# Performance work log

Measured on AMD Instinct MI355X. Metric: run time of the kernel, lower is better.

The kernel has to match this reference:

```python
import jax, jax.numpy as jnp
import numpy as np

NU = 8192   # num_users
NI = 8192   # num_items
B = 4096    # batch_size
D = 64      # embed_size
NS = 5      # num_scores


def _w(key, fan_in, fan_out):
    # xavier-uniform-like init
    lim = np.sqrt(6.0 / (fan_in + fan_out)).astype(np.float32)
    return jax.random.uniform(key, (fan_in, fan_out), jnp.float32, -lim, lim)


def setup_inputs() -> dict:
    key = jax.random.key(0)
    ks = jax.random.split(key, 32)
    z = lambda n: jnp.zeros((n,), jnp.float32)
    inp = {
        "batch_user": jax.random.randint(ks[0], (B,), 0, NU),
        "batch_item": jax.random.randint(ks[1], (B,), 0, NI),
        "R": jax.random.uniform(ks[2], (NU, NI), jnp.float32),
        "S": jax.random.uniform(ks[3], (NU, NU), jnp.float32),
        "U": _w(ks[4], NU, D),
        "V": _w(ks[5], NI, D),
        "w_r": _w(ks[6], NS, D), "b_r": z(D),
        "Wu0": _w(ks[7], 2 * D, D), "bu0": z(D), "Wu1": _w(ks[8], D, D), "bu1": z(D),
        "Wv0": _w(ks[9], 2 * D, D), "bv0": z(D), "Wv1": _w(ks[10], D, D), "bv1": z(D),
        "Wc0": _w(ks[11], 2 * D, D), "bc0": z(D), "Wc1": _w(ks[12], D, D), "bc1": z(D),
        "Wg0": _w(ks[13], 2 * D, D), "bg0": z(D), "Wg1": _w(ks[14], D, D), "bg1": z(D),
        "W_I": _w(ks[15], D, D), "b_I": z(D),
        "W_Sm": _w(ks[16], D, D), "b_Sm": z(D),
        "W1A": _w(ks[17], 2 * D, D), "b1A": z(D), "w2A": _w(ks[18], D, 1), "b2A": z(1),
        "W1B": _w(ks[19], 2 * D, D), "b1B": z(D), "w2B": _w(ks[20], D, 1), "b2B": z(1),
        "W1M": _w(ks[21], 2 * D, D), "b1M": z(D), "w2M": _w(ks[22], D, 1), "b2M": z(1),
        "W_Z": _w(ks[23], D, D), "b_Z": z(D),
    }
    return inp


def reference(batch_user, batch_item, R, S, U, V, w_r, b_r,
              Wu0, bu0, Wu1, bu1, Wv0, bv0, Wv1, bv1,
              Wc0, bc0, Wc1, bc1, Wg0, bg0, Wg1, bg1,
              W_I, b_I, W_Sm, b_Sm,
              W1A, b1A, w2A, b2A, W1B, b1B, w2B, b2B,
              W1M, b1M, w2M, b2M, W_Z, b_Z):
    relu = jax.nn.relu
    # rating embedding: e_r = Linear(num_scores->d) applied to vector [1..num_scores]
    e_r = jnp.arange(1, w_r.shape[0] + 1, dtype=w_r.dtype) @ w_r + b_r  # [d]
    Uc = jnp.concatenate([U, jnp.broadcast_to(e_r, U.shape)], axis=1)  # [NU, 2d]
    Vc = jnp.concatenate([V, jnp.broadcast_to(e_r, V.shape)], axis=1)  # [NI, 2d]
    # per-node MLP stacks (num_layer=2; layer0: 2d->d, layer1: d->d)
    Uh = relu(relu(Uc @ Wu0 + bu0) @ Wu1 + bu1)  # [NU, d]
    Vh = relu(relu(Vc @ Wv0 + bv0) @ Wv1 + bv1)  # [NI, d]
    Ub = Uh[batch_user]  # [B, d]
    Vb = Vh[batch_item]  # [B, d]
    # item-space attention A over batch, softmax along batch dim
    A = jax.nn.softmax(relu(jnp.concatenate([Vb, Ub], axis=1) @ W1A + b1A) @ w2A + b2A, axis=0)  # [B,1]
    # attention-weighted sparse-row aggregation over item embeddings
    H_I = relu(((R[batch_user] * A) @ Vh) @ W_I + b_I)  # [B, d]
    Bw = jax.nn.softmax(relu(jnp.concatenate([H_I, Ub], axis=1) @ W1B + b1B) @ w2B + b2B, axis=0)  # [B,1]
    H_S = relu(((S[batch_user] * Bw) @ Uh) @ W_Sm + b_Sm)  # [B, d]
    H = jnp.concatenate([H_I, H_S], axis=1)  # [B, 2d]
    H = relu(relu(H @ Wc0 + bc0) @ Wc1 + bc1)  # [B, d]
    M = jax.nn.softmax(relu(jnp.concatenate([Ub, Vb], axis=1) @ W1M + b1M) @ w2M + b2M, axis=0)  # [B,1]
    # R.T row-gather: columns of R for batch items -> [B, NU]
    Rt_b = jnp.take(R, batch_item, axis=1).T
    Z = relu(((Rt_b * M) @ Uh) @ W_Z + b_Z)  # [B, d]
    G = jnp.concatenate([H, Z], axis=1)  # [B, 2d]
    G = relu(relu(G @ Wg0 + bg0) @ Wg1 + bg1)  # [B, d]
    return G
```

## Files before the change

### kernel.cpp

```cpp
#include <hip/hip_runtime.h>
#include <stdint.h>


typedef short bf16x8 __attribute__((ext_vector_type(8)));
typedef float f32x4 __attribute__((ext_vector_type(4)));

#define NKZ    8
#define KLEN   1024
#define KITERS 32

__device__ __forceinline__ unsigned f2bf1(float f) {
    unsigned x = __float_as_uint(f);
    return (x + 0x7FFFu + ((x >> 16) & 1u)) >> 16;
}

__device__ __forceinline__ float wsum(float v) {
    #pragma unroll
    for (int o = 32; o; o >>= 1) v += __shfl_xor(v, o);
    return v;
}

__device__ __forceinline__ void block_softmax_stats(const float* __restrict__ s,
                                                    float& m, float& inv) {
    __shared__ float r1[4];
    __shared__ float r2[4];
    int t = threadIdx.x, lane = t & 63, wv = t >> 6;
    float lm = -3.4e38f;
    #pragma unroll
    for (int i = 0; i < 16; ++i) lm = fmaxf(lm, s[t + 256 * i]);
    #pragma unroll
    for (int o = 32; o; o >>= 1) lm = fmaxf(lm, __shfl_xor(lm, o));
    if (lane == 0) r1[wv] = lm;
    __syncthreads();
    m = fmaxf(fmaxf(r1[0], r1[1]), fmaxf(r1[2], r1[3]));
    float ls = 0.f;
    #pragma unroll
    for (int i = 0; i < 16; ++i) ls += __expf(s[t + 256 * i] - m);
    ls = wsum(ls);
    if (lane == 0) r2[wv] = ls;
    __syncthreads();
    inv = 1.f / (r2[0] + r2[1] + r2[2] + r2[3]);
}

__global__ __launch_bounds__(256) void k_mlp(
    const float* __restrict__ U, const float* __restrict__ V,
    const float* __restrict__ w_r, const float* __restrict__ b_r,
    const float* __restrict__ Wu0, const float* __restrict__ bu0,
    const float* __restrict__ Wu1, const float* __restrict__ bu1,
    const float* __restrict__ Wv0, const float* __restrict__ bv0,
    const float* __restrict__ Wv1, const float* __restrict__ bv1,
    float* __restrict__ Uh, float* __restrict__ Vh,
    unsigned short* __restrict__ Uhb, unsigned short* __restrict__ Vhb)
{
    int gt = blockIdx.x * 256 + threadIdx.x;
    int wid = gt >> 6;
    int lane = gt & 63;

    float er = b_r[lane];
    #pragma unroll
    for (int s = 0; s < 5; ++s) er += (float)(s + 1) * w_r[s * 64 + lane];

    const int isV = (wid >= 2048);
    const float* X  = isV ? V   : U;
    const float* W0 = isV ? Wv0 : Wu0;
    const float* B0 = isV ? bv0 : bu0;
    const float* W1 = isV ? Wv1 : Wu1;
    const float* B1 = isV ? bv1 : bu1;
    float* Hout          = isV ? Vh  : Uh;
    unsigned short* Hb   = isV ? Vhb : Uhb;
    int r0 = (wid & 2047) * 4;

    float x[4];
    #pragma unroll
    for (int j = 0; j < 4; ++j) x[j] = X[(r0 + j) * 64 + lane];

    float h0c = B0[lane];
    for (int k = 0; k < 64; ++k) h0c += __shfl(er, k) * W0[(64 + k) * 64 + lane];

    float h0[4];
    #pragma unroll
    for (int j = 0; j < 4; ++j) h0[j] = h0c;
    for (int k = 0; k < 64; ++k) {
        float wv = W0[k * 64 + lane];
        #pragma unroll
        for (int j = 0; j < 4; ++j) h0[j] += __shfl(x[j], k) * wv;
    }
    #pragma unroll
    for (int j = 0; j < 4; ++j) h0[j] = fmaxf(h0[j], 0.f);

    float h1[4];
    #pragma unroll
    for (int j = 0; j < 4; ++j) h1[j] = B1[lane];
    for (int k = 0; k < 64; ++k) {
        float wv = W1[k * 64 + lane];
        #pragma unroll
        for (int j = 0; j < 4; ++j) h1[j] += __shfl(h0[j], k) * wv;
    }
    #pragma unroll
    for (int j = 0; j < 4; ++j) {
        h1[j] = fmaxf(h1[j], 0.f);
        Hout[(r0 + j) * 64 + lane] = h1[j];
    }
    unsigned pw[2];
    #pragma unroll
    for (int q = 0; q < 2; ++q) pw[q] = f2bf1(h1[2*q]) | (f2bf1(h1[2*q+1]) << 16);
    unsigned short* dst = Hb + (size_t)(r0 >> 3) * 512 + (lane >> 4) * 128
                        + (lane & 15) * 8 + (r0 & 7);
    *(uint2*)dst = make_uint2(pw[0], pw[1]);
}

__global__ __launch_bounds__(256) void k_gemmQ(
    const float* __restrict__ R,
    const unsigned short* __restrict__ Uhb,
    float* __restrict__ Qp)
{
    __shared__ float lds[2][2048];
    const int tile = blockIdx.x & 127;
    const int kz   = blockIdx.x >> 7;
    const int i0 = tile * 64;
    const int u0 = kz * KLEN;
    const int t = threadIdx.x;
    const int w = t >> 6, l = t & 63, lg = l >> 4, lr = l & 15;

    f32x4 acc[4] = {};

    const float* gbase = R + ((size_t)u0 + (t >> 4)) * 8192 + i0 + (t & 15) * 4;

    #pragma unroll
    for (int q = 0; q < 2; ++q) {
        const float* g = gbase + (size_t)(q * 16) * 8192;
        __builtin_amdgcn_global_load_lds(
            (const __attribute__((address_space(1))) void*)g,
            (__attribute__((address_space(3))) void*)&lds[0][(q * 256 + t) * 4],
            16, 0, 0);
    }
    __syncthreads();

    const int iloc = w * 16 + lr;
    for (int s = 0; s < KITERS; ++s) {
        if (s + 1 < KITERS) {
            int nb = (s + 1) & 1;
            #pragma unroll
            for (int q = 0; q < 2; ++q) {
                const float* g = gbase + (size_t)((s + 1) * 32 + q * 16) * 8192;
                __builtin_amdgcn_global_load_lds(
                    (const __attribute__((address_space(1))) void*)g,
                    (__attribute__((address_space(3))) void*)&lds[nb][(q * 256 + t) * 4],
                    16, 0, 0);
            }
        }
        const float* Lb = lds[s & 1];
        float av[8];
        #pragma unroll
        for (int j = 0; j < 8; ++j) av[j] = Lb[(8 * lg + j) * 64 + iloc];
        union { bf16x8 v; unsigned u[4]; } af;
        #pragma unroll
        for (int q = 0; q < 4; ++q)
            af.u[q] = f2bf1(av[2*q]) | (f2bf1(av[2*q+1]) << 16);
        const unsigned short* bp = Uhb + (size_t)((u0 >> 3) + s * 4 + lg) * 512 + lr * 8;
        #pragma unroll
        for (int c = 0; c < 4; ++c) {
            bf16x8 bf = *(const bf16x8*)(bp + c * 128);
            acc[c] = __builtin_amdgcn_mfma_f32_16x16x32_bf16(af.v, bf, acc[c], 0, 0, 0);
        }
        __syncthreads();
    }

    float* out = Qp + (size_t)(kz * 8192 + tile * 64 + w * 16 + lg * 4) * 64 + lr;
    #pragma unroll
    for (int c = 0; c < 4; ++c) {
        #pragma unroll
        for (int j = 0; j < 4; ++j) out[j * 64 + c * 16] = acc[c][j];
    }
}

__global__ __launch_bounds__(256) void k_gemmP(
    const float* __restrict__ R, const float* __restrict__ S,
    const int* __restrict__ bu,
    const unsigned short* __restrict__ Uhb, const unsigned short* __restrict__ Vhb,
    float* __restrict__ PpI, float* __restrict__ PpS)
{
    const int gP = NKZ * 64;
    int bid = blockIdx.x;
    const int isS = bid >= gP;
    int q = isS ? bid - gP : bid;
    int tile = q & 63, kz = q >> 6;
    int tid = threadIdx.x;
    int w = tid >> 6, l = tid & 63;
    int lg = l >> 4, lr = l & 15;

    int brow = tile * 64 + w * 16 + lr;
    int ridx = bu[brow];
    const float* A = (isS ? S : R) + (size_t)ridx * 8192 + kz * KLEN + lg * 8;
    const unsigned short* Bb = (isS ? Uhb : Vhb)
                             + (size_t)((kz * KLEN) >> 3) * 512 + lr * 8;

    f32x4 acc[4] = {};
    f32x4 b0[4], b1[4];
    #pragma unroll
    for (int d = 0; d < 4; ++d) {
        b0[d] = ((const f32x4*)(A + d * 32))[0];
        b1[d] = ((const f32x4*)(A + d * 32))[1];
    }

    #pragma unroll 4
    for (int ks = 0; ks < KITERS - 4; ++ks) {
        const int slot = ks & 3;
        union { bf16x8 v; unsigned u[4]; } af;
        af.u[0] = f2bf1(b0[slot].x) | (f2bf1(b0[slot].y) << 16);
        af.u[1] = f2bf1(b0[slot].z) | (f2bf1(b0[slot].w) << 16);
        af.u[2] = f2bf1(b1[slot].x) | (f2bf1(b1[slot].y) << 16);
        af.u[3] = f2bf1(b1[slot].z) | (f2bf1(b1[slot].w) << 16);
        b0[slot] = ((const f32x4*)(A + (ks + 4) * 32))[0];
        b1[slot] = ((const f32x4*)(A + (ks + 4) * 32))[1];
        const unsigned short* bp = Bb + (size_t)(ks * 4 + lg) * 512;
        #pragma unroll
        for (int c = 0; c < 4; ++c) {
            bf16x8 bf = *(const bf16x8*)(bp + c * 128);
            acc[c] = __builtin_amdgcn_mfma_f32_16x16x32_bf16(af.v, bf, acc[c], 0, 0, 0);
        }
    }
    #pragma unroll
    for (int ks = KITERS - 4; ks < KITERS; ++ks) {
        const int slot = ks & 3;
        union { bf16x8 v; unsigned u[4]; } af;
        af.u[0] = f2bf1(b0[slot].x) | (f2bf1(b0[slot].y) << 16);
        af.u[1] = f2bf1(b0[slot].z) | (f2bf1(b0[slot].w) << 16);
        af.u[2] = f2bf1(b1[slot].x) | (f2bf1(b1[slot].y) << 16);
        af.u[3] = f2bf1(b1[slot].z) | (f2bf1(b1[slot].w) << 16);
        const unsigned short* bp = Bb + (size_t)(ks * 4 + lg) * 512;
        #pragma unroll
        for (int c = 0; c < 4; ++c) {
            bf16x8 bf = *(const bf16x8*)(bp + c * 128);
            acc[c] = __builtin_amdgcn_mfma_f32_16x16x32_bf16(af.v, bf, acc[c], 0, 0, 0);
        }
    }

    float* out = (isS ? PpS : PpI)
               + (size_t)(kz * 4096 + tile * 64 + w * 16 + lg * 4) * 64 + lr;
    #pragma unroll
    for (int c = 0; c < 4; ++c) {
        #pragma unroll
        for (int j = 0; j < 4; ++j) out[j * 64 + c * 16] = acc[c][j];
    }
}

__global__ __launch_bounds__(256) void k_scoreAM(
    const int* __restrict__ bu, const int* __restrict__ bi,
    const float* __restrict__ Uh, const float* __restrict__ Vh,
    const float* __restrict__ W1A, const float* __restrict__ b1A,
    const float* __restrict__ w2A, const float* __restrict__ b2A,
    const float* __restrict__ W1M, const float* __restrict__ b1M,
    const float* __restrict__ w2M, const float* __restrict__ b2M,
    float* __restrict__ sA, float* __restrict__ sM)
{
    int gt = blockIdx.x * 256 + threadIdx.x;
    int wid = gt >> 6, lane = gt & 63;
    int b0 = wid * 2;
    float ub[2], vb[2];
    #pragma unroll
    for (int j = 0; j < 2; ++j) {
        ub[j] = Uh[(size_t)bu[b0 + j] * 64 + lane];
        vb[j] = Vh[(size_t)bi[b0 + j] * 64 + lane];
    }
    float hA[2], hM[2];
    #pragma unroll
    for (int j = 0; j < 2; ++j) { hA[j] = b1A[lane]; hM[j] = b1M[lane]; }
    for (int k = 0; k < 64; ++k) {
        float wa0 = W1A[k * 64 + lane], wa1 = W1A[(64 + k) * 64 + lane];
        float wm0 = W1M[k * 64 + lane], wm1 = W1M[(64 + k) * 64 + lane];
        #pragma unroll
        for (int j = 0; j < 2; ++j) {
            float sv = __shfl(vb[j], k), su = __shfl(ub[j], k);
            hA[j] += sv * wa0 + su * wa1;
            hM[j] += su * wm0 + sv * wm1;
        }
    }
    float w2a = w2A[lane], w2m = w2M[lane];
    #pragma unroll
    for (int j = 0; j < 2; ++j) {
        float sa = wsum(fmaxf(hA[j], 0.f) * w2a);
        float sm = wsum(fmaxf(hM[j], 0.f) * w2m);
        if (lane == 0) { sA[b0 + j] = sa + b2A[0]; sM[b0 + j] = sm + b2M[0]; }
    }
}

__global__ __launch_bounds__(256) void k_HI_scoreB(
    const float* __restrict__ PpI, const float* __restrict__ sA,
    const int* __restrict__ bu, const float* __restrict__ Uh,
    const float* __restrict__ W_I, const float* __restrict__ b_I,
    const float* __restrict__ W1B, const float* __restrict__ b1B,
    const float* __restrict__ w2B, const float* __restrict__ b2B,
    float* __restrict__ HI, float* __restrict__ sB)
{
    float m, inv;
    block_softmax_stats(sA, m, inv);
    int wid = blockIdx.x * 4 + (threadIdx.x >> 6);
    int lane = threadIdx.x & 63;
    int b0 = wid * 2;
    float p[2];
    #pragma unroll
    for (int j = 0; j < 2; ++j) {
        int b = b0 + j;
        float a = 0.f;
        #pragma unroll
        for (int kz = 0; kz < NKZ; ++kz)
            a += PpI[(size_t)(kz * 4096 + b) * 64 + lane];
        p[j] = a * (__expf(sA[b] - m) * inv);
    }
    float h[2];
    #pragma unroll
    for (int j = 0; j < 2; ++j) h[j] = b_I[lane];
    for (int k = 0; k < 64; ++k) {
        float wv = W_I[k * 64 + lane];
        #pragma unroll
        for (int j = 0; j < 2; ++j) h[j] += __shfl(p[j], k) * wv;
    }
    float ub[2];
    #pragma unroll
    for (int j = 0; j < 2; ++j) {
        h[j] = fmaxf(h[j], 0.f);
        HI[(size_t)(b0 + j) * 64 + lane] = h[j];
        ub[j] = Uh[(size_t)bu[b0 + j] * 64 + lane];
    }
    float h2[2];
    #pragma unroll
    for (int j = 0; j < 2; ++j) h2[j] = b1B[lane];
    for (int k = 0; k < 64; ++k) {
        float w0 = W1B[k * 64 + lane], w1 = W1B[(64 + k) * 64 + lane];
        #pragma unroll
        for (int j = 0; j < 2; ++j) h2[j] += __shfl(h[j], k) * w0 + __shfl(ub[j], k) * w1;
    }
    float w2 = w2B[lane];
    #pragma unroll
    for (int j = 0; j < 2; ++j) {
        float sv = wsum(fmaxf(h2[j], 0.f) * w2);
        if (lane == 0) sB[b0 + j] = sv + b2B[0];
    }
}

__global__ __launch_bounds__(256) void k_HS_H(
    const float* __restrict__ PpS, const float* __restrict__ sB,
    const float* __restrict__ HI,
    const float* __restrict__ W_Sm, const float* __restrict__ b_Sm,
    const float* __restrict__ Wc0, const float* __restrict__ bc0,
    const float* __restrict__ Wc1, const float* __restrict__ bc1,
    float* __restrict__ Hout)
{
    float m, inv;
    block_softmax_stats(sB, m, inv);
    int wid = blockIdx.x * 4 + (threadIdx.x >> 6);
    int lane = threadIdx.x & 63;
    int b0 = wid * 2;
    float p[2];
    #pragma unroll
    for (int j = 0; j < 2; ++j) {
        int b = b0 + j;
        float a = 0.f;
        #pragma unroll
        for (int kz = 0; kz < NKZ; ++kz)
            a += PpS[(size_t)(kz * 4096 + b) * 64 + lane];
        p[j] = a * (__expf(sB[b] - m) * inv);
    }
    float hs[2];
    #pragma unroll
    for (int j = 0; j < 2; ++j) hs[j] = b_Sm[lane];
    for (int k = 0; k < 64; ++k) {
        float wv = W_Sm[k * 64 + lane];
        #pragma unroll
        for (int j = 0; j < 2; ++j) hs[j] += __shfl(p[j], k) * wv;
    }
    float hi[2];
    #pragma unroll
    for (int j = 0; j < 2; ++j) {
        hs[j] = fmaxf(hs[j], 0.f);
        hi[j] = HI[(size_t)(b0 + j) * 64 + lane];
    }
    float h0[2];
    #pragma unroll
    for (int j = 0; j < 2; ++j) h0[j] = bc0[lane];
    for (int k = 0; k < 64; ++k) {
        float w0 = Wc0[k * 64 + lane], w1 = Wc0[(64 + k) * 64 + lane];
        #pragma unroll
        for (int j = 0; j < 2; ++j) h0[j] += __shfl(hi[j], k) * w0 + __shfl(hs[j], k) * w1;
    }
    #pragma unroll
    for (int j = 0; j < 2; ++j) h0[j] = fmaxf(h0[j], 0.f);
    float h1[2];
    #pragma unroll
    for (int j = 0; j < 2; ++j) h1[j] = bc1[lane];
    for (int k = 0; k < 64; ++k) {
        float wv = Wc1[k * 64 + lane];
        #pragma unroll
        for (int j = 0; j < 2; ++j) h1[j] += __shfl(h0[j], k) * wv;
    }
    #pragma unroll
    for (int j = 0; j < 2; ++j) Hout[(size_t)(b0 + j) * 64 + lane] = fmaxf(h1[j], 0.f);
}

__global__ __launch_bounds__(256) void k_Z_G(
    const float* __restrict__ Qp, const float* __restrict__ sM,
    const int* __restrict__ bi, const float* __restrict__ H,
    const float* __restrict__ W_Z, const float* __restrict__ b_Z,
    const float* __restrict__ Wg0, const float* __restrict__ bg0,
    const float* __restrict__ Wg1, const float* __restrict__ bg1,
    float* __restrict__ G)
{
    float m, inv;
    block_softmax_stats(sM, m, inv);
    int wid = blockIdx.x * 4 + (threadIdx.x >> 6);
    int lane = threadIdx.x & 63;
    int b0 = wid * 2;
    float p[2];
    #pragma unroll
    for (int j = 0; j < 2; ++j) {
        int b = b0 + j;
        int it = bi[b];
        float a = 0.f;
        #pragma unroll
        for (int kz = 0; kz < NKZ; ++kz)
            a += Qp[(size_t)(kz * 8192 + it) * 64 + lane];
        p[j] = a * (__expf(sM[b] - m) * inv);
    }
    float z[2];
    #pragma unroll
    for (int j = 0; j < 2; ++j) z[j] = b_Z[lane];
    for (int k = 0; k < 64; ++k) {
        float wv = W_Z[k * 64 + lane];
        #pragma unroll
        for (int j = 0; j < 2; ++j) z[j] += __shfl(p[j], k) * wv;
    }
    float hr[2];
    #pragma unroll
    for (int j = 0; j < 2; ++j) {
        z[j] = fmaxf(z[j], 0.f);
        hr[j] = H[(size_t)(b0 + j) * 64 + lane];
    }
    float g0[2];
    #pragma unroll
    for (int j = 0; j < 2; ++j) g0[j] = bg0[lane];
    for (int k = 0; k < 64; ++k) {
        float w0 = Wg0[k * 64 + lane], w1 = Wg0[(64 + k) * 64 + lane];
        #pragma unroll
        for (int j = 0; j < 2; ++j) g0[j] += __shfl(hr[j], k) * w0 + __shfl(z[j], k) * w1;
    }
    #pragma unroll
    for (int j = 0; j < 2; ++j) g0[j] = fmaxf(g0[j], 0.f);
    float g1[2];
    #pragma unroll
    for (int j = 0; j < 2; ++j) g1[j] = bg1[lane];
    for (int k = 0; k < 64; ++k) {
        float wv = Wg1[k * 64 + lane];
        #pragma unroll
        for (int j = 0; j < 2; ++j) g1[j] += __shfl(g0[j], k) * wv;
    }
    #pragma unroll
    for (int j = 0; j < 2; ++j) G[(size_t)(b0 + j) * 64 + lane] = fmaxf(g1[j], 0.f);
}

extern "C" void kernel_launch(void* const* d_in, const int* in_sizes, int n_in,
                              void* d_out, int out_size, void* d_ws, size_t ws_size,
                              hipStream_t stream)
{
    (void)in_sizes; (void)n_in; (void)out_size; (void)ws_size;
    const int*   bu  = (const int*)  d_in[0];
    const int*   bi  = (const int*)  d_in[1];
    const float* R   = (const float*)d_in[2];
    const float* S   = (const float*)d_in[3];
    const float* U   = (const float*)d_in[4];
    const float* V   = (const float*)d_in[5];
    const float* w_r = (const float*)d_in[6];
    const float* b_r = (const float*)d_in[7];
    const float* Wu0 = (const float*)d_in[8];
    const float* bu0 = (const float*)d_in[9];
    const float* Wu1 = (const float*)d_in[10];
    const float* bu1 = (const float*)d_in[11];
    const float* Wv0 = (const float*)d_in[12];
    const float* bv0 = (const float*)d_in[13];
    const float* Wv1 = (const float*)d_in[14];
    const float* bv1 = (const float*)d_in[15];
    const float* Wc0 = (const float*)d_in[16];
    const float* bc0 = (const float*)d_in[17];
    const float* Wc1 = (const float*)d_in[18];
    const float* bc1 = (const float*)d_in[19];
    const float* Wg0 = (const float*)d_in[20];
    const float* bg0 = (const float*)d_in[21];
    const float* Wg1 = (const float*)d_in[22];
    const float* bg1 = (const float*)d_in[23];
    const float* W_I = (const float*)d_in[24];
    const float* b_I = (const float*)d_in[25];
    const float* W_Sm= (const float*)d_in[26];
    const float* b_Sm= (const float*)d_in[27];
    const float* W1A = (const float*)d_in[28];
    const float* b1A = (const float*)d_in[29];
    const float* w2A = (const float*)d_in[30];
    const float* b2A = (const float*)d_in[31];
    const float* W1B = (const float*)d_in[32];
    const float* b1B = (const float*)d_in[33];
    const float* w2B = (const float*)d_in[34];
    const float* b2B = (const float*)d_in[35];
    const float* W1M = (const float*)d_in[36];
    const float* b1M = (const float*)d_in[37];
    const float* w2M = (const float*)d_in[38];
    const float* b2M = (const float*)d_in[39];
    const float* W_Z = (const float*)d_in[40];
    const float* b_Z = (const float*)d_in[41];

    char* ws = (char*)d_ws;
    size_t off = 0;
    float*          Uh  = (float*)(ws + off);          off += 2ull << 20;
    float*          Vh  = (float*)(ws + off);          off += 2ull << 20;
    unsigned short* Uhb = (unsigned short*)(ws + off); off += 1ull << 20;
    unsigned short* Vhb = (unsigned short*)(ws + off); off += 1ull << 20;
    float*          PpI = (float*)(ws + off);          off += (size_t)NKZ << 20;
    float*          PpS = (float*)(ws + off);          off += (size_t)NKZ << 20;
    float*          Qp  = (float*)(ws + off);          off += (size_t)(2 * NKZ) << 20;
    float*          sA  = (float*)(ws + off);
    float*          sM  = sA + 4096;
    float*          sB  = sA + 8192;                   off += 3 * 4096 * 4 + 4096;
    float*          HI  = (float*)(ws + off);          off += 1ull << 20;
    float*          Hh  = (float*)(ws + off);

    k_mlp<<<1024, 256, 0, stream>>>(U, V, w_r, b_r, Wu0, bu0, Wu1, bu1,
                                    Wv0, bv0, Wv1, bv1, Uh, Vh, Uhb, Vhb);
    k_gemmQ<<<128 * NKZ, 256, 0, stream>>>(R, Uhb, Qp);
    k_gemmP<<<2 * NKZ * 64, 256, 0, stream>>>(R, S, bu, Uhb, Vhb, PpI, PpS);
    k_scoreAM<<<512, 256, 0, stream>>>(bu, bi, Uh, Vh, W1A, b1A, w2A, b2A,
                                       W1M, b1M, w2M, b2M, sA, sM);
    k_HI_scoreB<<<512, 256, 0, stream>>>(PpI, sA, bu, Uh, W_I, b_I,
                                         W1B, b1B, w2B, b2B, HI, sB);
    k_HS_H<<<512, 256, 0, stream>>>(PpS, sB, HI, W_Sm, b_Sm, Wc0, bc0, Wc1, bc1,
                                    Hh);
    k_Z_G<<<512, 256, 0, stream>>>(Qp, sM, bi, Hh, W_Z, b_Z, Wg0, bg0, Wg1, bg1,
                                   (float*)d_out);
}
```

Before: 224.1 us.

## Merge Q and P GEMMs into one launch with finer split-K

Folds the two split-K GEMM kernels (R^T·Uh over all items, and the gathered R/S rows times Vh/Uh) into one launch that branches on block index. The split-K factor rises from 8 to 16 for the P GEMMs and to 32 for the Q GEMM, and launch bounds request 4 blocks per CU. The intent is more blocks, better occupancy and overlap of the two memory-bound GEMMs, plus one fewer launch. In exchange the partial-sum buffers and the downstream reduction loops grow (Qp becomes 64 MB of partials), which adds write and read traffic.

```diff
diff --git a/kernel.cpp b/kernel.cpp
--- a/kernel.cpp
+++ b/kernel.cpp
@@ -5,9 +5,12 @@
 typedef short bf16x8 __attribute__((ext_vector_type(8)));
 typedef float f32x4 __attribute__((ext_vector_type(4)));
 
-#define NKZ    8
-#define KLEN   1024
-#define KITERS 32
+#define PKZ     16
+#define PKLEN   512
+#define PKITERS 16
+#define QKZ     32
+#define QKLEN   256
+#define QKITERS 8
 
 __device__ __forceinline__ unsigned f2bf1(float f) {
     unsigned x = __float_as_uint(f);
@@ -109,139 +112,132 @@
     *(uint2*)dst = make_uint2(pw[0], pw[1]);
 }
 
-__global__ __launch_bounds__(256) void k_gemmQ(
-    const float* __restrict__ R,
-    const unsigned short* __restrict__ Uhb,
-    float* __restrict__ Qp)
-{
-    __shared__ float lds[2][2048];
-    const int tile = blockIdx.x & 127;
-    const int kz   = blockIdx.x >> 7;
-    const int i0 = tile * 64;
-    const int u0 = kz * KLEN;
-    const int t = threadIdx.x;
-    const int w = t >> 6, l = t & 63, lg = l >> 4, lr = l & 15;
-
-    f32x4 acc[4] = {};
-
-    const float* gbase = R + ((size_t)u0 + (t >> 4)) * 8192 + i0 + (t & 15) * 4;
-
-    #pragma unroll
-    for (int q = 0; q < 2; ++q) {
-        const float* g = gbase + (size_t)(q * 16) * 8192;
-        __builtin_amdgcn_global_load_lds(
-            (const __attribute__((address_space(1))) void*)g,
-            (__attribute__((address_space(3))) void*)&lds[0][(q * 256 + t) * 4],
-            16, 0, 0);
-    }
-    __syncthreads();
-
-    const int iloc = w * 16 + lr;
-    for (int s = 0; s < KITERS; ++s) {
-        if (s + 1 < KITERS) {
-            int nb = (s + 1) & 1;
-            #pragma unroll
-            for (int q = 0; q < 2; ++q) {
-                const float* g = gbase + (size_t)((s + 1) * 32 + q * 16) * 8192;
-                __builtin_amdgcn_global_load_lds(
-                    (const __attribute__((address_space(1))) void*)g,
-                    (__attribute__((address_space(3))) void*)&lds[nb][(q * 256 + t) * 4],
-                    16, 0, 0);
-            }
-        }
-        const float* Lb = lds[s & 1];
-        float av[8];
-        #pragma unroll
-        for (int j = 0; j < 8; ++j) av[j] = Lb[(8 * lg + j) * 64 + iloc];
-        union { bf16x8 v; unsigned u[4]; } af;
-        #pragma unroll
-        for (int q = 0; q < 4; ++q)
-            af.u[q] = f2bf1(av[2*q]) | (f2bf1(av[2*q+1]) << 16);
-        const unsigned short* bp = Uhb + (size_t)((u0 >> 3) + s * 4 + lg) * 512 + lr * 8;
-        #pragma unroll
-        for (int c = 0; c < 4; ++c) {
-            bf16x8 bf = *(const bf16x8*)(bp + c * 128);
-            acc[c] = __builtin_amdgcn_mfma_f32_16x16x32_bf16(af.v, bf, acc[c], 0, 0, 0);
-        }
-        __syncthreads();
-    }
-
-    float* out = Qp + (size_t)(kz * 8192 + tile * 64 + w * 16 + lg * 4) * 64 + lr;
-    #pragma unroll
-    for (int c = 0; c < 4; ++c) {
-        #pragma unroll
-        for (int j = 0; j < 4; ++j) out[j * 64 + c * 16] = acc[c][j];
-    }
-}
-
-__global__ __launch_bounds__(256) void k_gemmP(
+__global__ __launch_bounds__(256, 4) void k_gemm(
     const float* __restrict__ R, const float* __restrict__ S,
     const int* __restrict__ bu,
     const unsigned short* __restrict__ Uhb, const unsigned short* __restrict__ Vhb,
-    float* __restrict__ PpI, float* __restrict__ PpS)
-{
-    const int gP = NKZ * 64;
-    int bid = blockIdx.x;
-    const int isS = bid >= gP;
-    int q = isS ? bid - gP : bid;
-    int tile = q & 63, kz = q >> 6;
-    int tid = threadIdx.x;
-    int w = tid >> 6, l = tid & 63;
-    int lg = l >> 4, lr = l & 15;
-
-    int brow = tile * 64 + w * 16 + lr;
-    int ridx = bu[brow];
-    const float* A = (isS ? S : R) + (size_t)ridx * 8192 + kz * KLEN + lg * 8;
-    const unsigned short* Bb = (isS ? Uhb : Vhb)
-                             + (size_t)((kz * KLEN) >> 3) * 512 + lr * 8;
+    float* __restrict__ PpI, float* __restrict__ PpS, float* __restrict__ Qp)
+{
+    __shared__ float lds[2][2048];
+    const int bid = blockIdx.x;
+    const int t = threadIdx.x;
+    const int w = t >> 6, l = t & 63, lg = l >> 4, lr = l & 15;
 
     f32x4 acc[4] = {};
-    f32x4 b0[4], b1[4];
-    #pragma unroll
-    for (int d = 0; d < 4; ++d) {
-        b0[d] = ((const f32x4*)(A + d * 32))[0];
-        b1[d] = ((const f32x4*)(A + d * 32))[1];
-    }
-
-    #pragma unroll 4
-    for (int ks = 0; ks < KITERS - 4; ++ks) {
-        const int slot = ks & 3;
-        union { bf16x8 v; unsigned u[4]; } af;
-        af.u[0] = f2bf1(b0[slot].x) | (f2bf1(b0[slot].y) << 16);
-        af.u[1] = f2bf1(b0[slot].z) | (f2bf1(b0[slot].w) << 16);
-        af.u[2] = f2bf1(b1[slot].x) | (f2bf1(b1[slot].y) << 16);
-        af.u[3] = f2bf1(b1[slot].z) | (f2bf1(b1[slot].w) << 16);
-        b0[slot] = ((const f32x4*)(A + (ks + 4) * 32))[0];
-        b1[slot] = ((const f32x4*)(A + (ks + 4) * 32))[1];
-        const unsigned short* bp = Bb + (size_t)(ks * 4 + lg) * 512;
+
+    if (bid < 2 * PKZ * 64) {
+        const int gP = PKZ * 64;
+        const int isS = bid >= gP;
+        int q = isS ? bid - gP : bid;
+        int tile = q & 63, kz = q >> 6;
+        int brow = tile * 64 + w * 16 + lr;
+        int ridx = bu[brow];
+        const float* A = (isS ? S : R) + (size_t)ridx * 8192 + kz * PKLEN + lg * 8;
+        const unsigned short* Bb = (isS ? Uhb : Vhb)
+                                 + (size_t)((kz * PKLEN) >> 3) * 512 + lr * 8;
+
+        f32x4 b0[4], b1[4];
+        #pragma unroll
+        for (int d = 0; d < 4; ++d) {
+            b0[d] = ((const f32x4*)(A + d * 32))[0];
+            b1[d] = ((const f32x4*)(A + d * 32))[1];
+        }
+
+        #pragma unroll 4
+        for (int ks = 0; ks < PKITERS - 4; ++ks) {
+            const int slot = ks & 3;
+            union { bf16x8 v; unsigned u[4]; } af;
+            af.u[0] = f2bf1(b0[slot].x) | (f2bf1(b0[slot].y) << 16);
+            af.u[1] = f2bf1(b0[slot].z) | (f2bf1(b0[slot].w) << 16);
+            af.u[2] = f2bf1(b1[slot].x) | (f2bf1(b1[slot].y) << 16);
+            af.u[3] = f2bf1(b1[slot].z) | (f2bf1(b1[slot].w) << 16);
+            b0[slot] = ((const f32x4*)(A + (ks + 4) * 32))[0];
+            b1[slot] = ((const f32x4*)(A + (ks + 4) * 32))[1];
+            const unsigned short* bp = Bb + (size_t)(ks * 4 + lg) * 512;
+            #pragma unroll
+            for (int c = 0; c < 4; ++c) {
+                bf16x8 bf = *(const bf16x8*)(bp + c * 128);
+                acc[c] = __builtin_amdgcn_mfma_f32_16x16x32_bf16(af.v, bf, acc[c], 0, 0, 0);
+            }
+        }
+        #pragma unroll
+        for (int ks = PKITERS - 4; ks < PKITERS; ++ks) {
+            const int slot = ks & 3;
+            union { bf16x8 v; unsigned u[4]; } af;
+            af.u[0] = f2bf1(b0[slot].x) | (f2bf1(b0[slot].y) << 16);
+            af.u[1] = f2bf1(b0[slot].z) | (f2bf1(b0[slot].w) << 16);
+            af.u[2] = f2bf1(b1[slot].x) | (f2bf1(b1[slot].y) << 16);
+            af.u[3] = f2bf1(b1[slot].z) | (f2bf1(b1[slot].w) << 16);
+            const unsigned short* bp = Bb + (size_t)(ks * 4 + lg) * 512;
+            #pragma unroll
+            for (int c = 0; c < 4; ++c) {
+                bf16x8 bf = *(const bf16x8*)(bp + c * 128);
+                acc[c] = __builtin_amdgcn_mfma_f32_16x16x32_bf16(af.v, bf, acc[c], 0, 0, 0);
+            }
+        }
+
+        float* out = (isS ? PpS : PpI)
+                   + (size_t)(kz * 4096 + tile * 64 + w * 16 + lg * 4) * 64 + lr;
         #pragma unroll
         for (int c = 0; c < 4; ++c) {
-            bf16x8 bf = *(const bf16x8*)(bp + c * 128);
-            acc[c] = __builtin_amdgcn_mfma_f32_16x16x32_bf16(af.v, bf, acc[c], 0, 0, 0);
-        }
-    }
-    #pragma unroll
-    for (int ks = KITERS - 4; ks < KITERS; ++ks) {
-        const int slot = ks & 3;
-        union { bf16x8 v; unsigned u[4]; } af;
-        af.u[0] = f2bf1(b0[slot].x) | (f2bf1(b0[slot].y) << 16);
-        af.u[1] = f2bf1(b0[slot].z) | (f2bf1(b0[slot].w) << 16);
-        af.u[2] = f2bf1(b1[slot].x) | (f2bf1(b1[slot].y) << 16);
-        af.u[3] = f2bf1(b1[slot].z) | (f2bf1(b1[slot].w) << 16);
-        const unsigned short* bp = Bb + (size_t)(ks * 4 + lg) * 512;
+            #pragma unroll
+            for (int j = 0; j < 4; ++j) out[j * 64 + c * 16] = acc[c][j];
+        }
+    } else {
+        int q = bid - 2 * PKZ * 64;
+        const int tile = q & 127;
+        const int kz   = q >> 7;
+        const int i0 = tile * 64;
+        const int u0 = kz * QKLEN;
+
+        const float* gbase = R + ((size_t)u0 + (t >> 4)) * 8192 + i0 + (t & 15) * 4;
+
+        #pragma unroll
+        for (int qq = 0; qq < 2; ++qq) {
+            const float* g = gbase + (size_t)(qq * 16) * 8192;
+            __builtin_amdgcn_global_load_lds(
+                (const __attribute__((address_space(1))) void*)g,
+                (__attribute__((address_space(3))) void*)&lds[0][(qq * 256 + t) * 4],
+                16, 0, 0);
+        }
+        __syncthreads();
+
+        const int iloc = w * 16 + lr;
+        for (int s = 0; s < QKITERS; ++s) {
+            if (s + 1 < QKITERS) {
+                int nb = (s + 1) & 1;
+                #pragma unroll
+                for (int qq = 0; qq < 2; ++qq) {
+                    const float* g = gbase + (size_t)((s + 1) * 32 + qq * 16) * 8192;
+                    __builtin_amdgcn_global_load_lds(
+                        (const __attribute__((address_space(1))) void*)g,
+                        (__attribute__((address_space(3))) void*)&lds[nb][(qq * 256 + t) * 4],
+                        16, 0, 0);
+                }
+            }
+            const float* Lb = lds[s & 1];
+            float av[8];
+            #pragma unroll
+            for (int j = 0; j < 8; ++j) av[j] = Lb[(8 * lg + j) * 64 + iloc];
+            union { bf16x8 v; unsigned u[4]; } af;
+            #pragma unroll
+            for (int qq = 0; qq < 4; ++qq)
+                af.u[qq] = f2bf1(av[2*qq]) | (f2bf1(av[2*qq+1]) << 16);
+            const unsigned short* bp = Uhb + (size_t)((u0 >> 3) + s * 4 + lg) * 512 + lr * 8;
+            #pragma unroll
+            for (int c = 0; c < 4; ++c) {
+                bf16x8 bf = *(const bf16x8*)(bp + c * 128);
+                acc[c] = __builtin_amdgcn_mfma_f32_16x16x32_bf16(af.v, bf, acc[c], 0, 0, 0);
+            }
+            __syncthreads();
+        }
+
+        float* out = Qp + (size_t)(kz * 8192 + tile * 64 + w * 16 + lg * 4) * 64 + lr;
         #pragma unroll
         for (int c = 0; c < 4; ++c) {
-            bf16x8 bf = *(const bf16x8*)(bp + c * 128);
-            acc[c] = __builtin_amdgcn_mfma_f32_16x16x32_bf16(af.v, bf, acc[c], 0, 0, 0);
-        }
-    }
-
-    float* out = (isS ? PpS : PpI)
-               + (size_t)(kz * 4096 + tile * 64 + w * 16 + lg * 4) * 64 + lr;
-    #pragma unroll
-    for (int c = 0; c < 4; ++c) {
-        #pragma unroll
-        for (int j = 0; j < 4; ++j) out[j * 64 + c * 16] = acc[c][j];
+            #pragma unroll
+            for (int j = 0; j < 4; ++j) out[j * 64 + c * 16] = acc[c][j];
+        }
     }
 }
 
@@ -303,8 +299,8 @@
     for (int j = 0; j < 2; ++j) {
         int b = b0 + j;
         float a = 0.f;
-        #pragma unroll
-        for (int kz = 0; kz < NKZ; ++kz)
+        #pragma unroll 8
+        for (int kz = 0; kz < PKZ; ++kz)
             a += PpI[(size_t)(kz * 4096 + b) * 64 + lane];
         p[j] = a * (__expf(sA[b] - m) * inv);
     }
@@ -357,8 +353,8 @@
     for (int j = 0; j < 2; ++j) {
         int b = b0 + j;
         float a = 0.f;
-        #pragma unroll
-        for (int kz = 0; kz < NKZ; ++kz)
+        #pragma unroll 8
+        for (int kz = 0; kz < PKZ; ++kz)
             a += PpS[(size_t)(kz * 4096 + b) * 64 + lane];
         p[j] = a * (__expf(sB[b] - m) * inv);
     }
@@ -417,8 +413,8 @@
         int b = b0 + j;
         int it = bi[b];
         float a = 0.f;
-        #pragma unroll
-        for (int kz = 0; kz < NKZ; ++kz)
+        #pragma unroll 8
+        for (int kz = 0; kz < QKZ; ++kz)
             a += Qp[(size_t)(kz * 8192 + it) * 64 + lane];
         p[j] = a * (__expf(sM[b] - m) * inv);
     }
@@ -512,9 +508,9 @@
     float*          Vh  = (float*)(ws + off);          off += 2ull << 20;
     unsigned short* Uhb = (unsigned short*)(ws + off); off += 1ull << 20;
     unsigned short* Vhb = (unsigned short*)(ws + off); off += 1ull << 20;
-    float*          PpI = (float*)(ws + off);          off += (size_t)NKZ << 20;
-    float*          PpS = (float*)(ws + off);          off += (size_t)NKZ << 20;
-    float*          Qp  = (float*)(ws + off);          off += (size_t)(2 * NKZ) << 20;
+    float*          PpI = (float*)(ws + off);          off += (size_t)PKZ << 20;
+    float*          PpS = (float*)(ws + off);          off += (size_t)PKZ << 20;
+    float*          Qp  = (float*)(ws + off);          off += (size_t)(2 * QKZ) << 20;
     float*          sA  = (float*)(ws + off);
     float*          sM  = sA + 4096;
     float*          sB  = sA + 8192;                   off += 3 * 4096 * 4 + 4096;
@@ -523,8 +519,8 @@
 
     k_mlp<<<1024, 256, 0, stream>>>(U, V, w_r, b_r, Wu0, bu0, Wu1, bu1,
                                     Wv0, bv0, Wv1, bv1, Uh, Vh, Uhb, Vhb);
-    k_gemmQ<<<128 * NKZ, 256, 0, stream>>>(R, Uhb, Qp);
-    k_gemmP<<<2 * NKZ * 64, 256, 0, stream>>>(R, S, bu, Uhb, Vhb, PpI, PpS);
+    k_gemm<<<2 * PKZ * 64 + 128 * QKZ, 256, 0, stream>>>(R, S, bu, Uhb, Vhb,
+                                                         PpI, PpS, Qp);
     k_scoreAM<<<512, 256, 0, stream>>>(bu, bi, Uh, Vh, W1A, b1A, w2A, b2A,
                                        W1M, b1M, w2M, b2M, sA, sM);
     k_HI_scoreB<<<512, 256, 0, stream>>>(PpI, sA, bu, Uh, W_I, b_I,
```

After: 235.3 us. 5.0% more time.
